# Kernel optimization log

Measured on AMD Instinct MI355X. Metric: run time of the kernel, lower is better.

Reference implementation:

```python
import jax, jax.numpy as jnp
import numpy as np

B, T, S, D, H = 8, 512, 512, 512, 8
DH = D // H
EPS = 1e-5


def _ln(x, g, b):
    m = x.mean(-1, keepdims=True)
    v = x.var(-1, keepdims=True)
    return (x - m) / jnp.sqrt(v + EPS) * g + b


def setup_inputs() -> dict:
    key = jax.random.key(0)
    ks = jax.random.split(key, 24)
    w = lambda k, shp: (jax.random.normal(k, shp, jnp.float32) * 0.02)
    causal = jnp.where(jnp.tril(jnp.ones((T, T), bool)), 0.0, -1e9).astype(jnp.float32)
    return {
        "tgt": jax.random.normal(ks[0], (B, T, D), jnp.float32),
        "memory": jax.random.normal(ks[1], (B, S, D), jnp.float32),
        "tgt_mask": causal,
        "gate": jax.random.uniform(ks[2], (T, D), jnp.float32),
        # self-attn params (torch MultiheadAttention packed in_proj layout)
        "sa_in_w": w(ks[3], (3 * D, D)), "sa_in_b": w(ks[4], (3 * D,)),
        "sa_out_w": w(ks[5], (D, D)), "sa_out_b": w(ks[6], (D,)),
        # cross-attn params
        "ca_in_w": w(ks[7], (3 * D, D)), "ca_in_b": w(ks[8], (3 * D,)),
        "ca_out_w": w(ks[9], (D, D)), "ca_out_b": w(ks[10], (D,)),
        # FFN
        "ff1_w": w(ks[11], (4 * D, D)), "ff1_b": w(ks[12], (4 * D,)),
        "ff2_w": w(ks[13], (D, 4 * D)), "ff2_b": w(ks[14], (D,)),
        # layernorms
        "ln1_g": jnp.ones((D,), jnp.float32), "ln1_b": jnp.zeros((D,), jnp.float32),
        "ln2_g": jnp.ones((D,), jnp.float32), "ln2_b": jnp.zeros((D,), jnp.float32),
        "ln3_g": jnp.ones((D,), jnp.float32), "ln3_b": jnp.zeros((D,), jnp.float32),
    }


def reference(tgt, memory, tgt_mask, gate,
              sa_in_w, sa_in_b, sa_out_w, sa_out_b,
              ca_in_w, ca_in_b, ca_out_w, ca_out_b,
              ff1_w, ff1_b, ff2_w, ff2_b,
              ln1_g, ln1_b, ln2_g, ln2_b, ln3_g, ln3_b):
    b, t, d = tgt.shape
    s = memory.shape[1]
    scale = 1.0 / jnp.sqrt(jnp.float32(DH))

    # ---- self attention (standard batched MHA, additive mask) ----
    wq, wk, wv = jnp.split(sa_in_w, 3, axis=0)
    bq, bk, bv = jnp.split(sa_in_b, 3, axis=0)
    q = ((tgt @ wq.T + bq).reshape(b, t, H, DH)) * scale
    k = (tgt @ wk.T + bk).reshape(b, t, H, DH)
    v = (tgt @ wv.T + bv).reshape(b, t, H, DH)
    scores = jnp.einsum('bthd,bshd->bhts', q, k) + tgt_mask  # (B,H,T,T)
    attn = jax.nn.softmax(scores, axis=-1)
    sa = jnp.einsum('bhts,bshd->bthd', attn, v).reshape(b, t, d) @ sa_out_w.T + sa_out_b
    x = _ln(tgt + sa, ln1_g, ln1_b)

    # ---- gated cross attention ----
    # Original: key_{b,t,s} = W_k(gate_t * memory_{b,s}) + b_k materialized as (B*T,S,D).
    # Faithful refactor: distribute W_k, fold (q W_k) with gate into the query side.
    cwq, cwk, cwv = jnp.split(ca_in_w, 3, axis=0)
    cbq, cbk, cbv = jnp.split(ca_in_b, 3, axis=0)
    cq = ((x @ cwq.T + cbq).reshape(b, t, H, DH)) * scale          # (B,T,H,dh)
    wk_h = cwk.reshape(H, DH, d)                                    # (H,dh,D)
    qW = jnp.einsum('bthe,hed->bthd', cq, wk_h)                     # (B,T,H,D)
    cscores = jnp.einsum('bthd,td,bsd->bhts', qW, gate, memory)     # (B,H,T,S)
    bk_h = cbk.reshape(H, DH)
    cscores = cscores + jnp.einsum('bthe,he->bht', cq, bk_h)[..., None]
    cattn = jax.nn.softmax(cscores, axis=-1)
    cv = (memory @ cwv.T + cbv).reshape(b, s, H, DH)
    ca = jnp.einsum('bhts,bshe->bthe', cattn, cv).reshape(b, t, d) @ ca_out_w.T + ca_out_b
    x = _ln(x + ca, ln2_g, ln2_b)

    # ---- FFN ----
    ff = jax.nn.relu(x @ ff1_w.T + ff1_b) @ ff2_w.T + ff2_b
    return _ln(x + ff, ln3_g, ln3_b)
```

## Files before the change

kernel.cpp:

```cpp
#include <hip/hip_runtime.h>
#include <hip/hip_bf16.h>

#define BB 8
#define TT 512
#define SS 512
#define DD 512
#define HH 8

typedef __attribute__((ext_vector_type(8))) short bf16x8;
typedef __attribute__((ext_vector_type(4))) float f32x4;
typedef unsigned short u16;

__device__ __forceinline__ u16 f2b(float f) {
    __hip_bfloat16 h = __float2bfloat16(f);
    return *reinterpret_cast<u16*>(&h);
}
__device__ __forceinline__ float b2f(u16 v) {
    unsigned int u = ((unsigned int)v) << 16;
    return __builtin_bit_cast(float, u);
}
__device__ __forceinline__ void g2lds16(const void* g, void* l) {
    __builtin_amdgcn_global_load_lds(
        (const __attribute__((address_space(1))) void*)g,
        (__attribute__((address_space(3))) void*)l, 16, 0, 0);
}
template <int N> __device__ __forceinline__ void waitvm();
template <> __device__ __forceinline__ void waitvm<0>() { asm volatile("s_waitcnt vmcnt(0)" ::: "memory"); }
template <> __device__ __forceinline__ void waitvm<6>() { asm volatile("s_waitcnt vmcnt(6)" ::: "memory"); }
template <> __device__ __forceinline__ void waitvm<8>() { asm volatile("s_waitcnt vmcnt(8)" ::: "memory"); }
template <> __device__ __forceinline__ void waitvm<9>() { asm volatile("s_waitcnt vmcnt(9)" ::: "memory"); }
__device__ __forceinline__ void barrier_raw() {
    asm volatile("" ::: "memory");
    __builtin_amdgcn_s_barrier();
    asm volatile("" ::: "memory");
}

struct CastSegs {
    const float* s[9];
    u16* d[9];
    int cum[10];
};
__global__ __launch_bounds__(256) void cast_multi(CastSegs sg) {
    const int total = sg.cum[9];
    for (int i = blockIdx.x * 256 + threadIdx.x; i < total; i += gridDim.x * 256) {
        int k = 0;
#pragma unroll
        for (int j = 1; j < 9; ++j) k += (i >= sg.cum[j]);
        const int loc = i - sg.cum[k];
        float4 v = ((const float4*)sg.s[k])[loc];
        ushort4 u;
        u.x = f2b(v.x); u.y = f2b(v.y); u.z = f2b(v.z); u.w = f2b(v.w);
        ((ushort4*)sg.d[k])[loc] = u;
    }
}

__global__ __launch_bounds__(256) void wkt_kernel(const float* __restrict__ w,
                                                  u16* __restrict__ o) {
    const int idx = blockIdx.x * 256 + threadIdx.x;
    const int h = idx >> 15, d = (idx >> 6) & 511, e = idx & 63;
    o[idx] = f2b(w[(size_t)(512 + h * 64 + e) * 512 + d]);
}

template <int TN, bool RELU, bool GATE>
__global__ __launch_bounds__(256) void gemm_bf16(
    const u16* __restrict__ A, int lda, long az,
    const u16* __restrict__ Bw, int ldb, long bz,
    const float* __restrict__ bias, const float* __restrict__ biasB,
    const float* __restrict__ gate,
    u16* __restrict__ C, int ldo, long cz,
    int K, float alpha, float alphaB) {
    __shared__ __align__(16) u16 As[2][128 * 64];
    __shared__ __align__(16) u16 Bs[2][TN * 64];
    const int tid = threadIdx.x;
    const int wave = tid >> 6, lane = tid & 63;
    const int lm = lane & 15, lg = lane >> 4;
    const int wm = wave >> 1, wn = wave & 1;
    const int m0 = blockIdx.y * 128, n0 = blockIdx.x * TN;
    A += (size_t)blockIdx.z * az;
    Bw += (size_t)blockIdx.z * bz;
    C += (size_t)blockIdx.z * cz;
    constexpr int FN = TN / 32;
    constexpr int LPS = 4 + TN / 32;

    f32x4 acc[4][FN];
#pragma unroll
    for (int mi = 0; mi < 4; ++mi)
#pragma unroll
        for (int ni = 0; ni < FN; ++ni) acc[mi][ni] = (f32x4){0.f, 0.f, 0.f, 0.f};

    const int srow = lane >> 3;
    const int sbyte = ((lane & 7) << 4) ^ (srow << 4);
    const int xk = (lm & 7) << 4;

    auto stage = [&](int buf, int kt) {
#pragma unroll
        for (int j = 0; j < 4; ++j) {
            const int r = wave * 32 + j * 8;
            g2lds16((const char*)(A + (size_t)(m0 + r + srow) * lda + kt) + sbyte,
                    (char*)As[buf] + (size_t)r * 128);
        }
#pragma unroll
        for (int j = 0; j < FN; ++j) {
            const int r = wave * (TN / 4) + j * 8;
            g2lds16((const char*)(Bw + (size_t)(n0 + r + srow) * ldb + kt) + sbyte,
                    (char*)Bs[buf] + (size_t)r * 128);
        }
    };

    stage(0, 0);
    const int NK = K >> 6;
    for (int t = 0; t < NK; ++t) {
        const int cur = t & 1;
        if (t + 1 < NK) { stage(cur ^ 1, (t + 1) << 6); waitvm<LPS>(); }
        else            { waitvm<0>(); }
        barrier_raw();
#pragma unroll
        for (int kh = 0; kh < 2; ++kh) {
            const int cb = kh * 64 + lg * 16;
            bf16x8 af[4], bfr[FN];
#pragma unroll
            for (int mi = 0; mi < 4; ++mi) {
                const int row = wm * 64 + mi * 16 + lm;
                af[mi] = *(const bf16x8*)((const char*)As[cur] + row * 128 + (cb ^ xk));
            }
#pragma unroll
            for (int ni = 0; ni < FN; ++ni) {
                const int row = wn * (TN / 2) + ni * 16 + lm;
                bfr[ni] = *(const bf16x8*)((const char*)Bs[cur] + row * 128 + (cb ^ xk));
            }
#pragma unroll
            for (int mi = 0; mi < 4; ++mi)
#pragma unroll
                for (int ni = 0; ni < FN; ++ni)
                    acc[mi][ni] = __builtin_amdgcn_mfma_f32_16x16x32_bf16(
                        af[mi], bfr[ni], acc[mi][ni], 0, 0, 0);
        }
        barrier_raw();
    }

    const float* bp = blockIdx.z ? biasB : bias;
    const float al = blockIdx.z ? alphaB : alpha;
#pragma unroll
    for (int mi = 0; mi < 4; ++mi)
#pragma unroll
        for (int ni = 0; ni < FN; ++ni)
#pragma unroll
            for (int r = 0; r < 4; ++r) {
                const int m = m0 + wm * 64 + mi * 16 + lg * 4 + r;
                const int n = n0 + wn * (TN / 2) + ni * 16 + lm;
                float v = acc[mi][ni][r];
                if constexpr (GATE) v *= gate[(size_t)(m & 511) * 512 + n];
                else                v = (v + bp[n]) * al;
                if constexpr (RELU) v = fmaxf(v, 0.f);
                C[(size_t)m * ldo + n] = f2b(v);
            }
}

__global__ __launch_bounds__(256) void flash_self(const u16* __restrict__ QKV,
                                                  u16* __restrict__ out) {
    const int t0 = blockIdx.x * 64, h = blockIdx.y, b = blockIdx.z;
    const int tid = threadIdx.x, wave = tid >> 6, lane = tid & 63;
    const int lm = lane & 15, lg = lane >> 4;
    __shared__ __align__(16) u16 Ks[32 * 64];
    __shared__ __align__(16) u16 Vt[64][40];
    __shared__ __align__(16) u16 P[4][16][40];

    const int tw = t0 + wave * 16;
    const size_t qrow = (size_t)(b * TT + tw + lm) * 1536 + h * 64;
    bf16x8 qf[2];
    qf[0] = *(const bf16x8*)(QKV + qrow + lg * 8);
    qf[1] = *(const bf16x8*)(QKV + qrow + 32 + lg * 8);

    float m_run[4], l_run[4];
    f32x4 oacc[4];
#pragma unroll
    for (int r = 0; r < 4; ++r) { m_run[r] = -3e38f; l_run[r] = 0.f; }
#pragma unroll
    for (int nt = 0; nt < 4; ++nt) oacc[nt] = (f32x4){0.f, 0.f, 0.f, 0.f};

    const int srow = lane >> 3, sbyte = ((lane & 7) << 4) ^ (srow << 4);
    const int xk = (lm & 7) << 4;
    const int smax = t0 + 64;
    for (int s0 = 0; s0 < smax; s0 += 32) {
        if (s0) __syncthreads();
        g2lds16((const char*)(QKV + (size_t)(b * TT + s0 + wave * 8 + srow) * 1536 +
                              512 + h * 64) + sbyte,
                (char*)Ks + wave * 1024);
        {
            const int s = tid & 31, d0 = (tid >> 5) * 8;
            bf16x8 vv = *(const bf16x8*)(QKV + (size_t)(b * TT + s0 + s) * 1536 +
                                         1024 + h * 64 + d0);
#pragma unroll
            for (int j = 0; j < 8; ++j) Vt[d0 + j][s] = (u16)vv[j];
        }
        __syncthreads();
        if (s0 <= tw + 15) {
            f32x4 sc0 = (f32x4){0.f, 0.f, 0.f, 0.f};
            f32x4 sc1 = (f32x4){0.f, 0.f, 0.f, 0.f};
#pragma unroll
            for (int f = 0; f < 2; ++f) {
                const int cb = f * 64 + lg * 16;
                bf16x8 k0 = *(const bf16x8*)((const char*)Ks + lm * 128 + (cb ^ xk));
                bf16x8 k1 = *(const bf16x8*)((const char*)Ks + (16 + lm) * 128 + (cb ^ xk));
                sc0 = __builtin_amdgcn_mfma_f32_16x16x32_bf16(qf[f], k0, sc0, 0, 0, 0);
                sc1 = __builtin_amdgcn_mfma_f32_16x16x32_bf16(qf[f], k1, sc1, 0, 0, 0);
            }
            float sv0[4], sv1[4], tm[4];
#pragma unroll
            for (int r = 0; r < 4; ++r) {
                const int t = tw + lg * 4 + r;
                sv0[r] = sc0[r] * 0.125f + ((s0 + lm) <= t ? 0.f : -1e9f);
                sv1[r] = sc1[r] * 0.125f + ((s0 + 16 + lm) <= t ? 0.f : -1e9f);
                tm[r] = fmaxf(sv0[r], sv1[r]);
            }
#pragma unroll
            for (int off = 1; off < 16; off <<= 1)
#pragma unroll
                for (int r = 0; r < 4; ++r) tm[r] = fmaxf(tm[r], __shfl_xor(tm[r], off));
            float fac[4], rs[4];
#pragma unroll
            for (int r = 0; r < 4; ++r) {
                const float mn = fmaxf(m_run[r], tm[r]);
                fac[r] = __expf(m_run[r] - mn);
                m_run[r] = mn;
                const float p0 = __expf(sv0[r] - mn);
                const float p1 = __expf(sv1[r] - mn);
                P[wave][lg * 4 + r][lm] = f2b(p0);
                P[wave][lg * 4 + r][16 + lm] = f2b(p1);
                rs[r] = p0 + p1;
            }
#pragma unroll
            for (int off = 1; off < 16; off <<= 1)
#pragma unroll
                for (int r = 0; r < 4; ++r) rs[r] += __shfl_xor(rs[r], off);
#pragma unroll
            for (int r = 0; r < 4; ++r) l_run[r] = l_run[r] * fac[r] + rs[r];
#pragma unroll
            for (int nt = 0; nt < 4; ++nt)
#pragma unroll
                for (int r = 0; r < 4; ++r) oacc[nt][r] *= fac[r];
            const bf16x8 pf = *(const bf16x8*)&P[wave][lm][lg * 8];
#pragma unroll
            for (int nt = 0; nt < 4; ++nt) {
                const bf16x8 vf = *(const bf16x8*)&Vt[nt * 16 + lm][lg * 8];
                oacc[nt] = __builtin_amdgcn_mfma_f32_16x16x32_bf16(pf, vf, oacc[nt], 0, 0, 0);
            }
        }
    }
#pragma unroll
    for (int nt = 0; nt < 4; ++nt)
#pragma unroll
        for (int r = 0; r < 4; ++r)
            out[(size_t)(b * TT + tw + lg * 4 + r) * DD + h * 64 + nt * 16 + lm] =
                f2b(oacc[nt][r] / l_run[r]);
}

__global__ __launch_bounds__(256) void flash_cross(
    const u16* __restrict__ QW, const u16* __restrict__ Kmem,
    const u16* __restrict__ CV, u16* __restrict__ out) {
    const int t0 = blockIdx.x * 64, h = blockIdx.y, b = blockIdx.z;
    const int tid = threadIdx.x, wave = tid >> 6, lane = tid & 63;
    const int lm = lane & 15, lg = lane >> 4;
    __shared__ __align__(16) u16 Ks[2][32 * 512];
    __shared__ __align__(16) u16 Vt[2][64][40];
    __shared__ __align__(16) u16 P[4][16][40];

    const int tw = t0 + wave * 16;
    const size_t qrow = (size_t)(b * TT + tw + lm) * 4096 + h * 512;
    bf16x8 qf[16];
#pragma unroll
    for (int f = 0; f < 16; ++f)
        qf[f] = *(const bf16x8*)(QW + qrow + f * 32 + lg * 8);

    float m_run[4], l_run[4];
    f32x4 oacc[4];
#pragma unroll
    for (int r = 0; r < 4; ++r) { m_run[r] = -3e38f; l_run[r] = 0.f; }
#pragma unroll
    for (int nt = 0; nt < 4; ++nt) oacc[nt] = (f32x4){0.f, 0.f, 0.f, 0.f};

    const int xk = (lm & 7) << 4;
    const int sV = tid & 31, d0 = (tid >> 5) * 8;

    auto stageK = [&](int buf, int s0) {
#pragma unroll
        for (int j = 0; j < 8; ++j) {
            const int row = wave * 8 + j;
            g2lds16((const char*)(Kmem + ((size_t)b * SS + s0 + row) * 512) +
                        ((lane * 16) ^ (j << 4)),
                    (char*)Ks[buf] + row * 1024);
        }
    };
    auto vload = [&](int s0) -> bf16x8 {
        return *(const bf16x8*)(CV + ((size_t)b * SS + s0 + sV) * 512 + h * 64 + d0);
    };

    stageK(0, 0);
    bf16x8 vrA = vload(0), vrB;
    for (int c = 0; c < 16; ++c) {
        const int cur = c & 1;
        if (c + 1 < 16) {
            stageK(cur ^ 1, (c + 1) * 32);
            vrB = vload((c + 1) * 32);
            waitvm<9>();
        } else {
            waitvm<0>();
        }
#pragma unroll
        for (int j = 0; j < 8; ++j) Vt[cur][d0 + j][sV] = (u16)vrA[j];
        asm volatile("s_waitcnt lgkmcnt(0)" ::: "memory");
        barrier_raw();
        f32x4 sc0 = (f32x4){0.f, 0.f, 0.f, 0.f};
        f32x4 sc1 = (f32x4){0.f, 0.f, 0.f, 0.f};
#pragma unroll
        for (int f = 0; f < 16; ++f) {
            const int cb = f * 64 + lg * 16;
            bf16x8 k0 = *(const bf16x8*)((const char*)Ks[cur] + lm * 1024 + (cb ^ xk));
            bf16x8 k1 = *(const bf16x8*)((const char*)Ks[cur] + (16 + lm) * 1024 + (cb ^ xk));
            sc0 = __builtin_amdgcn_mfma_f32_16x16x32_bf16(qf[f], k0, sc0, 0, 0, 0);
            sc1 = __builtin_amdgcn_mfma_f32_16x16x32_bf16(qf[f], k1, sc1, 0, 0, 0);
        }
        float sv0[4], sv1[4], tm[4];
#pragma unroll
        for (int r = 0; r < 4; ++r) {
            sv0[r] = sc0[r]; sv1[r] = sc1[r];
            tm[r] = fmaxf(sv0[r], sv1[r]);
        }
#pragma unroll
        for (int off = 1; off < 16; off <<= 1)
#pragma unroll
            for (int r = 0; r < 4; ++r) tm[r] = fmaxf(tm[r], __shfl_xor(tm[r], off));
        float fac[4], rs[4];
#pragma unroll
        for (int r = 0; r < 4; ++r) {
            const float mn = fmaxf(m_run[r], tm[r]);
            fac[r] = __expf(m_run[r] - mn);
            m_run[r] = mn;
            const float p0 = __expf(sv0[r] - mn);
            const float p1 = __expf(sv1[r] - mn);
            P[wave][lg * 4 + r][lm] = f2b(p0);
            P[wave][lg * 4 + r][16 + lm] = f2b(p1);
            rs[r] = p0 + p1;
        }
#pragma unroll
        for (int off = 1; off < 16; off <<= 1)
#pragma unroll
            for (int r = 0; r < 4; ++r) rs[r] += __shfl_xor(rs[r], off);
#pragma unroll
        for (int r = 0; r < 4; ++r) l_run[r] = l_run[r] * fac[r] + rs[r];
#pragma unroll
        for (int nt = 0; nt < 4; ++nt)
#pragma unroll
            for (int r = 0; r < 4; ++r) oacc[nt][r] *= fac[r];
        const bf16x8 pf = *(const bf16x8*)&P[wave][lm][lg * 8];
#pragma unroll
        for (int nt = 0; nt < 4; ++nt) {
            const bf16x8 vf = *(const bf16x8*)&Vt[cur][nt * 16 + lm][lg * 8];
            oacc[nt] = __builtin_amdgcn_mfma_f32_16x16x32_bf16(pf, vf, oacc[nt], 0, 0, 0);
        }
        barrier_raw();
        vrA = vrB;
    }
#pragma unroll
    for (int nt = 0; nt < 4; ++nt)
#pragma unroll
        for (int r = 0; r < 4; ++r)
            out[(size_t)(b * TT + tw + lg * 4 + r) * DD + h * 64 + nt * 16 + lm] =
                f2b(oacc[nt][r] / l_run[r]);
}

template <bool R1B>
__global__ __launch_bounds__(256) void add_ln(
    const void* __restrict__ R1v, const u16* __restrict__ R2,
    const float* __restrict__ g, const float* __restrict__ bta,
    float* __restrict__ outf, u16* __restrict__ outb) {
    const int row = blockIdx.x, tid = threadIdx.x;
    float x0, x1;
    if constexpr (R1B) {
        ushort2 a = ((const ushort2*)((const u16*)R1v + (size_t)row * DD))[tid];
        x0 = b2f(a.x); x1 = b2f(a.y);
    } else {
        float2 a = ((const float2*)((const float*)R1v + (size_t)row * DD))[tid];
        x0 = a.x; x1 = a.y;
    }
    ushort2 c = ((const ushort2*)(R2 + (size_t)row * DD))[tid];
    x0 += b2f(c.x); x1 += b2f(c.y);

    __shared__ float2 red[256];
    red[tid] = make_float2(x0 + x1, x0 * x0 + x1 * x1);
    __syncthreads();
#pragma unroll
    for (int o = 128; o > 0; o >>= 1) {
        if (tid < o) {
            red[tid].x += red[tid + o].x;
            red[tid].y += red[tid + o].y;
        }
        __syncthreads();
    }
    const float mean = red[0].x * (1.f / 512.f);
    const float var = red[0].y * (1.f / 512.f) - mean * mean;
    const float rstd = rsqrtf(var + 1e-5f);
    const int i = tid * 2;
    const float y0 = (x0 - mean) * rstd * g[i] + bta[i];
    const float y1 = (x1 - mean) * rstd * g[i + 1] + bta[i + 1];
    if (outf) ((float2*)(outf + (size_t)row * DD))[tid] = make_float2(y0, y1);
    if (outb) {
        ushort2 ub; ub.x = f2b(y0); ub.y = f2b(y1);
        ((ushort2*)(outb + (size_t)row * DD))[tid] = ub;
    }
}

extern "C" void kernel_launch(void* const* d_in, const int* in_sizes, int n_in,
                              void* d_out, int out_size, void* d_ws, size_t ws_size,
                              hipStream_t stream) {
    const float* tgt      = (const float*)d_in[0];
    const float* memory   = (const float*)d_in[1];
    const float* gate     = (const float*)d_in[3];
    const float* sa_in_w  = (const float*)d_in[4];
    const float* sa_in_b  = (const float*)d_in[5];
    const float* sa_out_w = (const float*)d_in[6];
    const float* sa_out_b = (const float*)d_in[7];
    const float* ca_in_w  = (const float*)d_in[8];
    const float* ca_in_b  = (const float*)d_in[9];
    const float* ca_out_w = (const float*)d_in[10];
    const float* ca_out_b = (const float*)d_in[11];
    const float* ff1_w    = (const float*)d_in[12];
    const float* ff1_b    = (const float*)d_in[13];
    const float* ff2_w    = (const float*)d_in[14];
    const float* ff2_b    = (const float*)d_in[15];
    const float* ln1_g    = (const float*)d_in[16];
    const float* ln1_b    = (const float*)d_in[17];
    const float* ln2_g    = (const float*)d_in[18];
    const float* ln2_b    = (const float*)d_in[19];
    const float* ln3_g    = (const float*)d_in[20];
    const float* ln3_b    = (const float*)d_in[21];

    u16* ws16     = (u16*)d_ws;
    u16* QKVb     = ws16;
    u16* sa_preb  = ws16 + 6291456;
    u16* PRJb     = ws16 + 8388608;
    u16* X1b      = ws16 + 10485760;
    u16* memb     = ws16 + 12582912;
    u16* CQb      = ws16 + 14680064;
    u16* CVb      = ws16 + 16777216;
    u16* QW       = ws16 + 18874368;
    u16* ca_preb  = ws16 + 35651584;
    u16* PRJ2b    = ws16 + 37748736;
    u16* X2b      = ws16 + 39845888;
    u16* HHb      = ws16 + 41943040;
    u16* F1b      = ws16 + 50331648;
    u16* Wreg     = ws16 + 52428800;
    u16* sa_in_wb = Wreg;
    u16* sa_out_wb= Wreg + 786432;
    u16* ca_wq_b  = Wreg + 1048576;
    u16* ca_wv_b  = Wreg + 1310720;
    u16* WkT      = Wreg + 1572864;
    u16* ca_out_wb= Wreg + 1835008;
    u16* ff1_wb   = Wreg + 2097152;
    u16* ff2_wb   = Wreg + 3145728;
    u16* tgtb     = ws16 + 56623104;
    float* outf   = (float*)d_out;

    const dim3 blk(256);

    CastSegs sg;
    sg.s[0]=tgt; sg.s[1]=memory; sg.s[2]=sa_in_w; sg.s[3]=sa_out_w;
    sg.s[4]=ca_in_w; sg.s[5]=ca_in_w + (size_t)1024*512; sg.s[6]=ca_out_w;
    sg.s[7]=ff1_w; sg.s[8]=ff2_w;
    sg.d[0]=tgtb; sg.d[1]=memb; sg.d[2]=sa_in_wb; sg.d[3]=sa_out_wb;
    sg.d[4]=ca_wq_b; sg.d[5]=ca_wv_b; sg.d[6]=ca_out_wb;
    sg.d[7]=ff1_wb; sg.d[8]=ff2_wb;
    {
        const int n4[9] = {524288,524288,196608,65536,65536,65536,65536,262144,262144};
        int c = 0;
        for (int i = 0; i < 9; ++i) { sg.cum[i] = c; c += n4[i]; }
        sg.cum[9] = c;
    }
    cast_multi<<<2048, blk, 0, stream>>>(sg);
    wkt_kernel<<<1024, blk, 0, stream>>>(ca_in_w, WkT);

    gemm_bf16<128,false,false><<<dim3(12,32,1), blk, 0, stream>>>(
        tgtb,512,0, sa_in_wb,512,0, sa_in_b,sa_in_b,nullptr,
        QKVb,1536,0, 512, 1.f,1.f);
    flash_self<<<dim3(8,8,8), blk, 0, stream>>>(QKVb, sa_preb);
    gemm_bf16<64,false,false><<<dim3(8,32,1), blk, 0, stream>>>(
        sa_preb,512,0, sa_out_wb,512,0, sa_out_b,sa_out_b,nullptr,
        PRJb,512,0, 512, 1.f,1.f);
    add_ln<false><<<4096, blk, 0, stream>>>(tgt, PRJb, ln1_g, ln1_b, nullptr, X1b);
    gemm_bf16<64,false,false><<<dim3(8,32,2), blk, 0, stream>>>(
        X1b,512,2097152, ca_wq_b,512,262144, ca_in_b, ca_in_b+1024, nullptr,
        CQb,512,2097152, 512, 0.125f, 1.f);
    gemm_bf16<64,false,true><<<dim3(8,32,8), blk, 0, stream>>>(
        CQb,512,64, WkT,64,32768, nullptr,nullptr,gate,
        QW,4096,512, 64, 1.f,1.f);
    flash_cross<<<dim3(8,8,8), blk, 0, stream>>>(QW, memb, CVb, ca_preb);
    gemm_bf16<64,false,false><<<dim3(8,32,1), blk, 0, stream>>>(
        ca_preb,512,0, ca_out_wb,512,0, ca_out_b,ca_out_b,nullptr,
        PRJ2b,512,0, 512, 1.f,1.f);
    add_ln<true><<<4096, blk, 0, stream>>>(X1b, PRJ2b, ln2_g, ln2_b, nullptr, X2b);
    gemm_bf16<128,true,false><<<dim3(16,32,1), blk, 0, stream>>>(
        X2b,512,0, ff1_wb,512,0, ff1_b,ff1_b,nullptr,
        HHb,2048,0, 512, 1.f,1.f);
    gemm_bf16<64,false,false><<<dim3(8,32,1), blk, 0, stream>>>(
        HHb,2048,0, ff2_wb,2048,0, ff2_b,ff2_b,nullptr,
        F1b,512,0, 2048, 1.f,1.f);
    add_ln<true><<<4096, blk, 0, stream>>>(X2b, F1b, ln3_g, ln3_b, outf, nullptr);

    (void)in_sizes; (void)n_in; (void)out_size; (void)ws_size;
}
```

Baseline: 218.2 us.

## Use 64x64 GEMM tiles and two query blocks per wave in cross attention

The GEMM kernel gains a template parameter for the M tile, so the narrow N=512 projections and FFN2 run with 64x64 tiles on twice as many blocks. Cross-attention flash now runs 128-thread blocks in which each wave processes 32 query rows as two 16-row groups. Each K fragment read from LDS is reused for two MFMA row groups, and each thread transposes twice as much of V. The aim is better occupancy for the small GEMMs and less LDS traffic per FLOP in cross attention, at the cost of more registers per wave (two Q fragment sets and two accumulator sets) and smaller GEMM tiles with less reuse.

Measured after the change: 219.6 us. Within noise of the previous version (+0.6%).

```diff
diff --git a/kernel.cpp b/kernel.cpp
--- a/kernel.cpp
+++ b/kernel.cpp
@@ -25,10 +25,11 @@
         (__attribute__((address_space(3))) void*)l, 16, 0, 0);
 }
 template <int N> __device__ __forceinline__ void waitvm();
-template <> __device__ __forceinline__ void waitvm<0>() { asm volatile("s_waitcnt vmcnt(0)" ::: "memory"); }
-template <> __device__ __forceinline__ void waitvm<6>() { asm volatile("s_waitcnt vmcnt(6)" ::: "memory"); }
-template <> __device__ __forceinline__ void waitvm<8>() { asm volatile("s_waitcnt vmcnt(8)" ::: "memory"); }
-template <> __device__ __forceinline__ void waitvm<9>() { asm volatile("s_waitcnt vmcnt(9)" ::: "memory"); }
+template <> __device__ __forceinline__ void waitvm<0>()  { asm volatile("s_waitcnt vmcnt(0)" ::: "memory"); }
+template <> __device__ __forceinline__ void waitvm<4>()  { asm volatile("s_waitcnt vmcnt(4)" ::: "memory"); }
+template <> __device__ __forceinline__ void waitvm<6>()  { asm volatile("s_waitcnt vmcnt(6)" ::: "memory"); }
+template <> __device__ __forceinline__ void waitvm<8>()  { asm volatile("s_waitcnt vmcnt(8)" ::: "memory"); }
+template <> __device__ __forceinline__ void waitvm<18>() { asm volatile("s_waitcnt vmcnt(18)" ::: "memory"); }
 __device__ __forceinline__ void barrier_raw() {
     asm volatile("" ::: "memory");
     __builtin_amdgcn_s_barrier();
@@ -61,7 +62,7 @@
     o[idx] = f2b(w[(size_t)(512 + h * 64 + e) * 512 + d]);
 }
 
-template <int TN, bool RELU, bool GATE>
+template <int TM, int TN, bool RELU, bool GATE>
 __global__ __launch_bounds__(256) void gemm_bf16(
     const u16* __restrict__ A, int lda, long az,
     const u16* __restrict__ Bw, int ldb, long bz,
@@ -69,22 +70,23 @@
     const float* __restrict__ gate,
     u16* __restrict__ C, int ldo, long cz,
     int K, float alpha, float alphaB) {
-    __shared__ __align__(16) u16 As[2][128 * 64];
+    __shared__ __align__(16) u16 As[2][TM * 64];
     __shared__ __align__(16) u16 Bs[2][TN * 64];
     const int tid = threadIdx.x;
     const int wave = tid >> 6, lane = tid & 63;
     const int lm = lane & 15, lg = lane >> 4;
     const int wm = wave >> 1, wn = wave & 1;
-    const int m0 = blockIdx.y * 128, n0 = blockIdx.x * TN;
+    const int m0 = blockIdx.y * TM, n0 = blockIdx.x * TN;
     A += (size_t)blockIdx.z * az;
     Bw += (size_t)blockIdx.z * bz;
     C += (size_t)blockIdx.z * cz;
+    constexpr int MI = TM / 32;
     constexpr int FN = TN / 32;
-    constexpr int LPS = 4 + TN / 32;
-
-    f32x4 acc[4][FN];
-#pragma unroll
-    for (int mi = 0; mi < 4; ++mi)
+    constexpr int LPS = MI + FN;
+
+    f32x4 acc[MI][FN];
+#pragma unroll
+    for (int mi = 0; mi < MI; ++mi)
 #pragma unroll
         for (int ni = 0; ni < FN; ++ni) acc[mi][ni] = (f32x4){0.f, 0.f, 0.f, 0.f};
 
@@ -94,8 +96,8 @@
 
     auto stage = [&](int buf, int kt) {
 #pragma unroll
-        for (int j = 0; j < 4; ++j) {
-            const int r = wave * 32 + j * 8;
+        for (int j = 0; j < MI; ++j) {
+            const int r = wave * (TM / 4) + j * 8;
             g2lds16((const char*)(A + (size_t)(m0 + r + srow) * lda + kt) + sbyte,
                     (char*)As[buf] + (size_t)r * 128);
         }
@@ -117,10 +119,10 @@
 #pragma unroll
         for (int kh = 0; kh < 2; ++kh) {
             const int cb = kh * 64 + lg * 16;
-            bf16x8 af[4], bfr[FN];
-#pragma unroll
-            for (int mi = 0; mi < 4; ++mi) {
-                const int row = wm * 64 + mi * 16 + lm;
+            bf16x8 af[MI], bfr[FN];
+#pragma unroll
+            for (int mi = 0; mi < MI; ++mi) {
+                const int row = wm * (TM / 2) + mi * 16 + lm;
                 af[mi] = *(const bf16x8*)((const char*)As[cur] + row * 128 + (cb ^ xk));
             }
 #pragma unroll
@@ -129,7 +131,7 @@
                 bfr[ni] = *(const bf16x8*)((const char*)Bs[cur] + row * 128 + (cb ^ xk));
             }
 #pragma unroll
-            for (int mi = 0; mi < 4; ++mi)
+            for (int mi = 0; mi < MI; ++mi)
 #pragma unroll
                 for (int ni = 0; ni < FN; ++ni)
                     acc[mi][ni] = __builtin_amdgcn_mfma_f32_16x16x32_bf16(
@@ -141,12 +143,12 @@
     const float* bp = blockIdx.z ? biasB : bias;
     const float al = blockIdx.z ? alphaB : alpha;
 #pragma unroll
-    for (int mi = 0; mi < 4; ++mi)
+    for (int mi = 0; mi < MI; ++mi)
 #pragma unroll
         for (int ni = 0; ni < FN; ++ni)
 #pragma unroll
             for (int r = 0; r < 4; ++r) {
-                const int m = m0 + wm * 64 + mi * 16 + lg * 4 + r;
+                const int m = m0 + wm * (TM / 2) + mi * 16 + lg * 4 + r;
                 const int n = n0 + wn * (TN / 2) + ni * 16 + lm;
                 float v = acc[mi][ni][r];
                 if constexpr (GATE) v *= gate[(size_t)(m & 511) * 512 + n];
@@ -255,7 +257,7 @@
                 f2b(oacc[nt][r] / l_run[r]);
 }
 
-__global__ __launch_bounds__(256) void flash_cross(
+__global__ __launch_bounds__(128, 2) void flash_cross(
     const u16* __restrict__ QW, const u16* __restrict__ Kmem,
     const u16* __restrict__ CV, u16* __restrict__ out) {
     const int t0 = blockIdx.x * 64, h = blockIdx.y, b = blockIdx.z;
@@ -263,110 +265,142 @@
     const int lm = lane & 15, lg = lane >> 4;
     __shared__ __align__(16) u16 Ks[2][32 * 512];
     __shared__ __align__(16) u16 Vt[2][64][40];
-    __shared__ __align__(16) u16 P[4][16][40];
-
-    const int tw = t0 + wave * 16;
-    const size_t qrow = (size_t)(b * TT + tw + lm) * 4096 + h * 512;
-    bf16x8 qf[16];
-#pragma unroll
-    for (int f = 0; f < 16; ++f)
-        qf[f] = *(const bf16x8*)(QW + qrow + f * 32 + lg * 8);
-
-    float m_run[4], l_run[4];
-    f32x4 oacc[4];
-#pragma unroll
-    for (int r = 0; r < 4; ++r) { m_run[r] = -3e38f; l_run[r] = 0.f; }
-#pragma unroll
-    for (int nt = 0; nt < 4; ++nt) oacc[nt] = (f32x4){0.f, 0.f, 0.f, 0.f};
+    __shared__ __align__(16) u16 P[2][32][40];
+
+    const int tq = t0 + wave * 32;
+    const size_t qrowA = (size_t)(b * TT + tq + lm) * 4096 + h * 512;
+    const size_t qrowB = qrowA + (size_t)16 * 4096;
+    bf16x8 qfA[16], qfB[16];
+#pragma unroll
+    for (int f = 0; f < 16; ++f) {
+        qfA[f] = *(const bf16x8*)(QW + qrowA + f * 32 + lg * 8);
+        qfB[f] = *(const bf16x8*)(QW + qrowB + f * 32 + lg * 8);
+    }
+
+    float mA[4], lA[4], mB[4], lB[4];
+    f32x4 oA[4], oB[4];
+#pragma unroll
+    for (int r = 0; r < 4; ++r) { mA[r] = -3e38f; lA[r] = 0.f; mB[r] = -3e38f; lB[r] = 0.f; }
+#pragma unroll
+    for (int nt = 0; nt < 4; ++nt) { oA[nt] = (f32x4){0.f,0.f,0.f,0.f}; oB[nt] = (f32x4){0.f,0.f,0.f,0.f}; }
 
     const int xk = (lm & 7) << 4;
-    const int sV = tid & 31, d0 = (tid >> 5) * 8;
+    const int sV = tid & 31, dV = (tid >> 5) * 16;
 
     auto stageK = [&](int buf, int s0) {
 #pragma unroll
-        for (int j = 0; j < 8; ++j) {
-            const int row = wave * 8 + j;
+        for (int j = 0; j < 16; ++j) {
+            const int row = wave * 16 + j;
             g2lds16((const char*)(Kmem + ((size_t)b * SS + s0 + row) * 512) +
-                        ((lane * 16) ^ (j << 4)),
+                        ((lane * 16) ^ ((j & 7) << 4)),
                     (char*)Ks[buf] + row * 1024);
         }
     };
-    auto vload = [&](int s0) -> bf16x8 {
-        return *(const bf16x8*)(CV + ((size_t)b * SS + s0 + sV) * 512 + h * 64 + d0);
+    auto vload0 = [&](int s0) -> bf16x8 {
+        return *(const bf16x8*)(CV + ((size_t)b * SS + s0 + sV) * 512 + h * 64 + dV);
     };
+    auto vload1 = [&](int s0) -> bf16x8 {
+        return *(const bf16x8*)(CV + ((size_t)b * SS + s0 + sV) * 512 + h * 64 + dV + 8);
+    };
 
     stageK(0, 0);
-    bf16x8 vrA = vload(0), vrB;
+    bf16x8 vr0 = vload0(0), vr1 = vload1(0), vn0, vn1;
     for (int c = 0; c < 16; ++c) {
         const int cur = c & 1;
         if (c + 1 < 16) {
             stageK(cur ^ 1, (c + 1) * 32);
-            vrB = vload((c + 1) * 32);
-            waitvm<9>();
+            vn0 = vload0((c + 1) * 32);
+            vn1 = vload1((c + 1) * 32);
+            waitvm<18>();
         } else {
             waitvm<0>();
         }
 #pragma unroll
-        for (int j = 0; j < 8; ++j) Vt[cur][d0 + j][sV] = (u16)vrA[j];
+        for (int j = 0; j < 8; ++j) {
+            Vt[cur][dV + j][sV] = (u16)vr0[j];
+            Vt[cur][dV + 8 + j][sV] = (u16)vr1[j];
+        }
         asm volatile("s_waitcnt lgkmcnt(0)" ::: "memory");
         barrier_raw();
-        f32x4 sc0 = (f32x4){0.f, 0.f, 0.f, 0.f};
-        f32x4 sc1 = (f32x4){0.f, 0.f, 0.f, 0.f};
+        f32x4 sA0 = (f32x4){0.f,0.f,0.f,0.f}, sA1 = (f32x4){0.f,0.f,0.f,0.f};
+        f32x4 sB0 = (f32x4){0.f,0.f,0.f,0.f}, sB1 = (f32x4){0.f,0.f,0.f,0.f};
 #pragma unroll
         for (int f = 0; f < 16; ++f) {
             const int cb = f * 64 + lg * 16;
             bf16x8 k0 = *(const bf16x8*)((const char*)Ks[cur] + lm * 1024 + (cb ^ xk));
             bf16x8 k1 = *(const bf16x8*)((const char*)Ks[cur] + (16 + lm) * 1024 + (cb ^ xk));
-            sc0 = __builtin_amdgcn_mfma_f32_16x16x32_bf16(qf[f], k0, sc0, 0, 0, 0);
-            sc1 = __builtin_amdgcn_mfma_f32_16x16x32_bf16(qf[f], k1, sc1, 0, 0, 0);
-        }
-        float sv0[4], sv1[4], tm[4];
+            sA0 = __builtin_amdgcn_mfma_f32_16x16x32_bf16(qfA[f], k0, sA0, 0, 0, 0);
+            sA1 = __builtin_amdgcn_mfma_f32_16x16x32_bf16(qfA[f], k1, sA1, 0, 0, 0);
+            sB0 = __builtin_amdgcn_mfma_f32_16x16x32_bf16(qfB[f], k0, sB0, 0, 0, 0);
+            sB1 = __builtin_amdgcn_mfma_f32_16x16x32_bf16(qfB[f], k1, sB1, 0, 0, 0);
+        }
+        float tmA[4], tmB[4];
 #pragma unroll
         for (int r = 0; r < 4; ++r) {
-            sv0[r] = sc0[r]; sv1[r] = sc1[r];
-            tm[r] = fmaxf(sv0[r], sv1[r]);
+            tmA[r] = fmaxf(sA0[r], sA1[r]);
+            tmB[r] = fmaxf(sB0[r], sB1[r]);
         }
 #pragma unroll
         for (int off = 1; off < 16; off <<= 1)
 #pragma unroll
-            for (int r = 0; r < 4; ++r) tm[r] = fmaxf(tm[r], __shfl_xor(tm[r], off));
-        float fac[4], rs[4];
+            for (int r = 0; r < 4; ++r) {
+                tmA[r] = fmaxf(tmA[r], __shfl_xor(tmA[r], off));
+                tmB[r] = fmaxf(tmB[r], __shfl_xor(tmB[r], off));
+            }
+        float facA[4], facB[4], rsA[4], rsB[4];
 #pragma unroll
         for (int r = 0; r < 4; ++r) {
-            const float mn = fmaxf(m_run[r], tm[r]);
-            fac[r] = __expf(m_run[r] - mn);
-            m_run[r] = mn;
-            const float p0 = __expf(sv0[r] - mn);
-            const float p1 = __expf(sv1[r] - mn);
-            P[wave][lg * 4 + r][lm] = f2b(p0);
-            P[wave][lg * 4 + r][16 + lm] = f2b(p1);
-            rs[r] = p0 + p1;
+            const float mnA = fmaxf(mA[r], tmA[r]);
+            facA[r] = __expf(mA[r] - mnA); mA[r] = mnA;
+            const float pA0 = __expf(sA0[r] - mnA);
+            const float pA1 = __expf(sA1[r] - mnA);
+            P[wave][lg * 4 + r][lm] = f2b(pA0);
+            P[wave][lg * 4 + r][16 + lm] = f2b(pA1);
+            rsA[r] = pA0 + pA1;
+            const float mnB = fmaxf(mB[r], tmB[r]);
+            facB[r] = __expf(mB[r] - mnB); mB[r] = mnB;
+            const float pB0 = __expf(sB0[r] - mnB);
+            const float pB1 = __expf(sB1[r] - mnB);
+            P[wave][16 + lg * 4 + r][lm] = f2b(pB0);
+            P[wave][16 + lg * 4 + r][16 + lm] = f2b(pB1);
+            rsB[r] = pB0 + pB1;
         }
 #pragma unroll
         for (int off = 1; off < 16; off <<= 1)
 #pragma unroll
-            for (int r = 0; r < 4; ++r) rs[r] += __shfl_xor(rs[r], off);
-#pragma unroll
-        for (int r = 0; r < 4; ++r) l_run[r] = l_run[r] * fac[r] + rs[r];
+            for (int r = 0; r < 4; ++r) {
+                rsA[r] += __shfl_xor(rsA[r], off);
+                rsB[r] += __shfl_xor(rsB[r], off);
+            }
+#pragma unroll
+        for (int r = 0; r < 4; ++r) {
+            lA[r] = lA[r] * facA[r] + rsA[r];
+            lB[r] = lB[r] * facB[r] + rsB[r];
+        }
 #pragma unroll
         for (int nt = 0; nt < 4; ++nt)
 #pragma unroll
-            for (int r = 0; r < 4; ++r) oacc[nt][r] *= fac[r];
-        const bf16x8 pf = *(const bf16x8*)&P[wave][lm][lg * 8];
+            for (int r = 0; r < 4; ++r) { oA[nt][r] *= facA[r]; oB[nt][r] *= facB[r]; }
+        const bf16x8 pfA = *(const bf16x8*)&P[wave][lm][lg * 8];
+        const bf16x8 pfB = *(const bf16x8*)&P[wave][16 + lm][lg * 8];
 #pragma unroll
         for (int nt = 0; nt < 4; ++nt) {
             const bf16x8 vf = *(const bf16x8*)&Vt[cur][nt * 16 + lm][lg * 8];
-            oacc[nt] = __builtin_amdgcn_mfma_f32_16x16x32_bf16(pf, vf, oacc[nt], 0, 0, 0);
+            oA[nt] = __builtin_amdgcn_mfma_f32_16x16x32_bf16(pfA, vf, oA[nt], 0, 0, 0);
+            oB[nt] = __builtin_amdgcn_mfma_f32_16x16x32_bf16(pfB, vf, oB[nt], 0, 0, 0);
         }
         barrier_raw();
-        vrA = vrB;
+        vr0 = vn0; vr1 = vn1;
     }
 #pragma unroll
     for (int nt = 0; nt < 4; ++nt)
 #pragma unroll
-        for (int r = 0; r < 4; ++r)
-            out[(size_t)(b * TT + tw + lg * 4 + r) * DD + h * 64 + nt * 16 + lm] =
-                f2b(oacc[nt][r] / l_run[r]);
+        for (int r = 0; r < 4; ++r) {
+            out[(size_t)(b * TT + tq + lg * 4 + r) * DD + h * 64 + nt * 16 + lm] =
+                f2b(oA[nt][r] / lA[r]);
+            out[(size_t)(b * TT + tq + 16 + lg * 4 + r) * DD + h * 64 + nt * 16 + lm] =
+                f2b(oB[nt][r] / lB[r]);
+        }
 }
 
 template <bool R1B>
@@ -479,29 +513,29 @@
     cast_multi<<<2048, blk, 0, stream>>>(sg);
     wkt_kernel<<<1024, blk, 0, stream>>>(ca_in_w, WkT);
 
-    gemm_bf16<128,false,false><<<dim3(12,32,1), blk, 0, stream>>>(
+    gemm_bf16<128,128,false,false><<<dim3(12,32,1), blk, 0, stream>>>(
         tgtb,512,0, sa_in_wb,512,0, sa_in_b,sa_in_b,nullptr,
         QKVb,1536,0, 512, 1.f,1.f);
     flash_self<<<dim3(8,8,8), blk, 0, stream>>>(QKVb, sa_preb);
-    gemm_bf16<64,false,false><<<dim3(8,32,1), blk, 0, stream>>>(
+    gemm_bf16<64,64,false,false><<<dim3(8,64,1), blk, 0, stream>>>(
         sa_preb,512,0, sa_out_wb,512,0, sa_out_b,sa_out_b,nullptr,
         PRJb,512,0, 512, 1.f,1.f);
     add_ln<false><<<4096, blk, 0, stream>>>(tgt, PRJb, ln1_g, ln1_b, nullptr, X1b);
-    gemm_bf16<64,false,false><<<dim3(8,32,2), blk, 0, stream>>>(
+    gemm_bf16<64,64,false,false><<<dim3(8,64,2), blk, 0, stream>>>(
         X1b,512,2097152, ca_wq_b,512,262144, ca_in_b, ca_in_b+1024, nullptr,
         CQb,512,2097152, 512, 0.125f, 1.f);
-    gemm_bf16<64,false,true><<<dim3(8,32,8), blk, 0, stream>>>(
+    gemm_bf16<64,64,false,true><<<dim3(8,64,8), blk, 0, stream>>>(
         CQb,512,64, WkT,64,32768, nullptr,nullptr,gate,
         QW,4096,512, 64, 1.f,1.f);
-    flash_cross<<<dim3(8,8,8), blk, 0, stream>>>(QW, memb, CVb, ca_preb);
-    gemm_bf16<64,false,false><<<dim3(8,32,1), blk, 0, stream>>>(
+    flash_cross<<<dim3(8,8,8), dim3(128), 0, stream>>>(QW, memb, CVb, ca_preb);
+    gemm_bf16<64,64,false,false><<<dim3(8,64,1), blk, 0, stream>>>(
         ca_preb,512,0, ca_out_wb,512,0, ca_out_b,ca_out_b,nullptr,
         PRJ2b,512,0, 512, 1.f,1.f);
     add_ln<true><<<4096, blk, 0, stream>>>(X1b, PRJ2b, ln2_g, ln2_b, nullptr, X2b);
-    gemm_bf16<128,true,false><<<dim3(16,32,1), blk, 0, stream>>>(
+    gemm_bf16<128,128,true,false><<<dim3(16,32,1), blk, 0, stream>>>(
         X2b,512,0, ff1_wb,512,0, ff1_b,ff1_b,nullptr,
         HHb,2048,0, 512, 1.f,1.f);
-    gemm_bf16<64,false,false><<<dim3(8,32,1), blk, 0, stream>>>(
+    gemm_bf16<64,64,false,false><<<dim3(8,64,1), blk, 0, stream>>>(
         HHb,2048,0, ff2_wb,2048,0, ff2_b,ff2_b,nullptr,
         F1b,512,0, 2048, 1.f,1.f);
     add_ln<true><<<4096, blk, 0, stream>>>(X2b, F1b, ln3_g, ln3_b, outf, nullptr);
```
